# Performance work log

Hardware: AMD Instinct MI355X
Metric: run time of the kernel (lower is better)

## Reference

```python
import jax, jax.numpy as jnp
import numpy as np
from jax import lax

DG = 8          # deformable groups
KH = KW = 3
K = KH * KW
PAD = 1


def conv3x3(x, w, b):
    # x: (B,C,H,W), w: (O,C,3,3) -> SAME conv, stride 1
    y = lax.conv_general_dilated(x, w, (1, 1), ((PAD, PAD), (PAD, PAD)),
                                 dimension_numbers=('NCHW', 'OIHW', 'NCHW'))
    return y + b[None, :, None, None]


def lrelu(x):
    return jnp.where(x >= 0, x, 0.1 * x)


def modulated_deform_conv(x, offset, mask, w, b):
    """DCNv2 semantics: stride=1, pad=1, dilation=1, groups=1.
    x: (B,C,H,W); offset: (B, 2*DG*K, H, W); mask: (B, DG*K, H, W) (already sigmoided);
    w: (O, C, 3, 3); b: (O,).
    Offset channel layout per CUDA kernel: (DG, K, 2[y,x]).
    """
    B, C, H, W = x.shape
    cg = C // DG
    off = offset.reshape(B, DG, K, 2, H, W)
    dy, dx = off[:, :, :, 0], off[:, :, :, 1]            # (B,DG,K,H,W)

    ky, kx = jnp.meshgrid(jnp.arange(KH), jnp.arange(KW), indexing='ij')
    ky = ky.reshape(K).astype(x.dtype)
    kx = kx.reshape(K).astype(x.dtype)
    base_y = jnp.arange(H, dtype=x.dtype)[None, :, None] - PAD + ky[:, None, None]  # (K,H,1)
    base_x = jnp.arange(W, dtype=x.dtype)[None, None, :] - PAD + kx[:, None, None]  # (K,1,W)
    py = dy + base_y                                     # (B,DG,K,H,W)
    px = dx + base_x

    y0 = jnp.floor(py)
    x0 = jnp.floor(px)
    wy = py - y0
    wx = px - x0
    y0i = y0.astype(jnp.int32)
    x0i = x0.astype(jnp.int32)

    xg = x.reshape(B, DG, cg, H * W)

    def gather(yi, xi):
        valid = ((yi >= 0) & (yi < H) & (xi >= 0) & (xi < W)).astype(x.dtype)
        idx = jnp.clip(yi, 0, H - 1) * W + jnp.clip(xi, 0, W - 1)   # (B,DG,K,H,W)
        idxf = idx.reshape(B, DG, 1, K * H * W)
        vals = jnp.take_along_axis(xg, jnp.broadcast_to(idxf, (B, DG, cg, K * H * W)), axis=3)
        return vals.reshape(B, DG, cg, K, H, W) * valid[:, :, None]

    samp = gather(y0i, x0i) * ((1 - wy) * (1 - wx))[:, :, None]
    samp = samp + gather(y0i, x0i + 1) * ((1 - wy) * wx)[:, :, None]
    samp = samp + gather(y0i + 1, x0i) * (wy * (1 - wx))[:, :, None]
    samp = samp + gather(y0i + 1, x0i + 1) * (wy * wx)[:, :, None]

    samp = samp * mask.reshape(B, DG, 1, K, H, W)        # modulated
    wr = w.reshape(w.shape[0], DG, cg, K)
    out = jnp.einsum('odck,bdckhw->bohw', wr, samp)
    return out + b[None, :, None, None]


def dcn_pack(x, feat, off_w, off_b, w, b):
    # conv_offset on `feat` -> (B, 3*DG*K, H, W); chunk into o1,o2,mask
    out = conv3x3(feat, off_w, off_b)
    o1, o2, m = jnp.split(out, 3, axis=1)
    offset = jnp.concatenate([o1, o2], axis=1)
    mask = jax.nn.sigmoid(m)
    return modulated_deform_conv(x, offset, mask, w, b)


def setup_inputs() -> dict:
    key = jax.random.key(0)
    ks = jax.random.split(key, 24)
    B, C, H, W = 4, 64, 192, 192
    nf = C

    def wconv(k, o, i, s=0.02):
        return jax.random.normal(k, (o, i, 3, 3), jnp.float32) * s

    inp = {
        'nbr_l1': jax.random.normal(ks[0], (B, C, H, W), jnp.float32),
        'ref_l1': jax.random.normal(ks[1], (B, C, H, W), jnp.float32),
        'oc1_w': wconv(ks[2], nf, 2 * nf), 'oc1_b': jnp.zeros((nf,), jnp.float32),
        'oc2_w': wconv(ks[3], nf, nf), 'oc2_b': jnp.zeros((nf,), jnp.float32),
        'dcn1_off_w': wconv(ks[4], 3 * DG * K, nf, 0.01), 'dcn1_off_b': jnp.zeros((3 * DG * K,), jnp.float32),
        'dcn1_w': wconv(ks[5], nf, nf), 'dcn1_b': jnp.zeros((nf,), jnp.float32),
        'fc_w': wconv(ks[6], nf, nf), 'fc_b': jnp.zeros((nf,), jnp.float32),
        'cas1_w': wconv(ks[7], nf, 2 * nf), 'cas1_b': jnp.zeros((nf,), jnp.float32),
        'cas2_w': wconv(ks[8], nf, nf), 'cas2_b': jnp.zeros((nf,), jnp.float32),
        'casd_off_w': wconv(ks[9], 3 * DG * K, nf, 0.01), 'casd_off_b': jnp.zeros((3 * DG * K,), jnp.float32),
        'casd_w': wconv(ks[10], nf, nf), 'casd_b': jnp.zeros((nf,), jnp.float32),
    }
    return inp


def reference(nbr_l1, ref_l1, oc1_w, oc1_b, oc2_w, oc2_b,
              dcn1_off_w, dcn1_off_b, dcn1_w, dcn1_b, fc_w, fc_b,
              cas1_w, cas1_b, cas2_w, cas2_b,
              casd_off_w, casd_off_b, casd_w, casd_b):
    offset = jnp.concatenate([nbr_l1, ref_l1], axis=1)
    offset = lrelu(conv3x3(offset, oc1_w, oc1_b))
    offset = lrelu(conv3x3(offset, oc2_w, oc2_b))
    feat = dcn_pack(nbr_l1, offset, dcn1_off_w, dcn1_off_b, dcn1_w, dcn1_b)
    feat = conv3x3(feat, fc_w, fc_b)                     # no activation (matches source)
    offset = jnp.concatenate([feat, ref_l1], axis=1)
    offset = lrelu(conv3x3(lrelu(conv3x3(offset, cas1_w, cas1_b)), cas2_w, cas2_b))
    feat = lrelu(dcn_pack(feat, offset, casd_off_w, casd_off_b, casd_w, casd_b))
    return feat
```

## Files before the change

### kernel.cpp

```cpp
#include <hip/hip_runtime.h>
#include <hip/hip_bf16.h>
#include <math.h>

typedef __hip_bfloat16 bf16;
typedef float  floatx16 __attribute__((ext_vector_type(16)));
typedef short  short8   __attribute__((ext_vector_type(8)));

#define Bn 4
#define NF 64
#define Hn 192
#define Wn 192
#define HWn (Hn*Wn)

#define WA_OC1  0
#define WA_OC2  73728
#define WA_FC   110592
#define WA_CAS1 147456
#define WA_CAS2 221184
#define WA_D1O  258048
#define WA_CDO  405504
#define WP_D1   552960
#define WP_CD   589824
#define B_OC1  0
#define B_OC2  64
#define B_FC   128
#define B_CAS1 192
#define B_CAS2 256
#define B_D1O  320
#define B_CDO  536
#define B_D1P  752
#define B_CDP  816
#define BIAS_OFF  1024
#define WPOOL_OFF 5120
#define BUF_OFF   1261568
#define FEAT_BYTES 18874368

#define WROWS 12
#define WCOLS 12
#define WSTR  72
#define SSTR2 152

__device__ __forceinline__ float b2f(bf16 v){ return __bfloat162float(v); }
__device__ __forceinline__ bf16  f2b(float v){ return __float2bfloat16(v); }
__device__ __forceinline__ float us2f(unsigned short u){ return __uint_as_float(((unsigned)u) << 16); }
__device__ __forceinline__ float ld(const void* p, size_t i, int f32){
    if (f32) return ((const float*)p)[i];
    return b2f(((const bf16*)p)[i]);
}

union B8 { uint2 u2[2]; uint4 u4; short8 s8; };
union V8 { uint4 u4; unsigned short us[8]; bf16 h[8]; };
union V4 { uint2 u2; bf16 h[4]; };

struct P20 { const void* p[20]; int n[20]; };

__global__ void detect_bias(P20 a, int* __restrict__ flags, float* __restrict__ bp){
    __shared__ int sf[20];
    int t = threadIdx.x;
    if (t < 20){
        const unsigned short* u = (const unsigned short*)a.p[t];
        int n = a.n[t]; if (n > 512) n = 512;
        int f32 = 0;
        for (int i = 0; i < n; ++i){
            float v = __uint_as_float(((unsigned)u[i]) << 16);
            if (!(fabsf(v) < 1e3f)) f32 = 1;
        }
        sf[t] = f32; flags[t] = f32;
    }
    __syncthreads();
    const int src[9] = {3,5,11,13,15,7,17,9,19};
    const int off[9] = {B_OC1,B_OC2,B_FC,B_CAS1,B_CAS2,B_D1O,B_CDO,B_D1P,B_CDP};
    const int sz[9]  = {64,64,64,64,64,216,216,64,64};
    for (int s = 0; s < 9; ++s)
        if (t < sz[s]) bp[off[s] + t] = ld(a.p[src[s]], t, sf[src[s]]);
}

__global__ void prep_weights(P20 a, const int* __restrict__ flags, bf16* __restrict__ wp)
{
    const int srcI[9] = {2,4,10,12,14,6,16,8,18};
    const int dstO[9] = {WA_OC1,WA_OC2,WA_FC,WA_CAS1,WA_CAS2,WA_D1O,WA_CDO,WP_D1,WP_CD};
    const int cinA[9] = {128,64,64,128,64,64,64,0,0};
    const int coutA[9]= {64,64,64,64,64,216,216,0,0};
    const int nblk[9] = {288,144,144,288,144,576,576,144,144};

    int bx = blockIdx.x;
    int j = 0, base = 0;
    while (j < 8 && bx >= base + nblk[j]){ base += nblk[j]; ++j; }
    int idx = (bx - base)*256 + threadIdx.x;
    const void* src = a.p[srcI[j]];
    const int f = flags[srcI[j]];
    bf16* dst = wp + dstO[j];

    int jj = idx & 7;
    int ko = (idx>>3) & 1;
    int mm = (idx>>4) & 31;
    int rest = idx >> 9;
    if (cinA[j]){
        int KK = cinA[j] >> 4;
        int kk = rest % KK; rest /= KK;
        int tap = rest % 9;
        int ocb = rest / 9;
        int oc = ocb*32 + mm;
        int ci = kk*16 + ko*8 + jj;
        float v = 0.f;
        if (oc < coutA[j]) v = ld(src, ((size_t)oc*cinA[j] + ci)*9 + tap, f);
        dst[idx] = f2b(v);
    } else {
        int kk = rest % 36;
        int ocb = rest / 36;
        int oc = ocb*32 + mm;
        int kp   = kk*16 + ko*8 + jj;
        int slot = kp >> 3;
        int cg   = kp & 7;
        int dg   = slot / 9;
        int tap  = slot - dg*9;
        int k    = (dg*8 + cg)*9 + tap;
        dst[idx] = f2b(ld(src, (size_t)oc*576 + k, f));
    }
}

__global__ __launch_bounds__(256)
void pack_x(const void* __restrict__ src, const int* __restrict__ flags, int fi,
            bf16* __restrict__ dst)
{
    __shared__ bf16 s[64*65];
    const int b    = blockIdx.y;
    const int pix0 = blockIdx.x * 64;
    const int t    = threadIdx.x;
    const int f    = (fi >= 0) ? flags[fi] : 0;

    const int px8 = (t & 7) * 8;
    const int ci0 = t >> 3;
#pragma unroll
    for (int it = 0; it < 2; ++it){
        int ci = ci0 + it*32;
        size_t g = ((size_t)b*NF + ci)*HWn + pix0 + px8;
        if (f){
            float4 a0 = *(const float4*)((const float*)src + g);
            float4 a1 = *(const float4*)((const float*)src + g + 4);
            bf16* sp = &s[ci*65 + px8];
            sp[0]=f2b(a0.x); sp[1]=f2b(a0.y); sp[2]=f2b(a0.z); sp[3]=f2b(a0.w);
            sp[4]=f2b(a1.x); sp[5]=f2b(a1.y); sp[6]=f2b(a1.z); sp[7]=f2b(a1.w);
        } else {
            V8 v; v.u4 = *(const uint4*)((const bf16*)src + g);
            bf16* sp = &s[ci*65 + px8];
#pragma unroll
            for (int j = 0; j < 8; ++j) sp[j] = v.h[j];
        }
    }
    __syncthreads();

    const int px  = t >> 2;
    const int ch0 = (t & 3) * 16;
    V8 o0, o1;
#pragma unroll
    for (int j = 0; j < 8; ++j){
        o0.h[j] = s[(ch0 + j)*65 + px];
        o1.h[j] = s[(ch0 + 8 + j)*65 + px];
    }
    bf16* dp = dst + ((size_t)b*HWn + pix0 + px)*64 + ch0;
    *(uint4*)(dp)     = o0.u4;
    *(uint4*)(dp + 8) = o1.u4;
}

template<int KK, int NOCB>
__global__ __launch_bounds__(256, 2)
void conv_mfma(const bf16* __restrict__ inA, const bf16* __restrict__ inB,
               const bf16* __restrict__ wA, const float* __restrict__ bias,
               bf16* __restrict__ out, int ACT)
{
    constexpr int CinT  = KK*16;
    constexpr int ciPad = CinT + 4;
    constexpr int CH8   = CinT/8;
    constexpr int CSH   = (KK==4)?3:4;
    extern __shared__ __align__(16) char smem_raw[];
    bf16* s_in = (bf16*)smem_raw;

    const int b  = blockIdx.z;
    const int bx = blockIdx.x;
    const int ty = bx/3, tx = bx - ty*3;
    const int h0 = ty*2, x0 = tx*64;
    const int tid = threadIdx.x;

    for (int r = 0; r < 4; ++r){
        const int y = h0 - 1 + r;
        const bool yv = (unsigned)y < (unsigned)Hn;
        const size_t rb = ((size_t)b*HWn + (size_t)y*Wn)*64;
        for (int e = tid; e < 66*CH8; e += 256){
            const int c   = e >> CSH;
            const int ch8 = e & (CH8-1);
            const int x = x0 - 1 + c;
            B8 v; v.u4 = make_uint4(0,0,0,0);
            if (yv && (unsigned)x < (unsigned)Wn){
                if (KK==8 && ch8 >= 8) v.u4 = *(const uint4*)(inB + rb + (size_t)x*64 + (ch8-8)*8);
                else                   v.u4 = *(const uint4*)(inA + rb + (size_t)x*64 + ch8*8);
            }
            bf16* dp = &s_in[(size_t)(r*66 + c)*ciPad + ch8*8];
            *(uint2*)(dp)     = v.u2[0];
            *(uint2*)(dp + 4) = v.u2[1];
        }
    }
    __syncthreads();

    const int w    = tid >> 6;
    const int lane = tid & 63;
    const int m    = lane & 31;
    const int half = lane >> 5;
    const int och  = (w >> 1) * 32;
    const int rw   = (w & 1);
    const int gpx0 = (h0 + rw)*Wn + x0;

#pragma unroll
    for (int ot = 0; ot < NOCB; ++ot){
        const int ocb = ot*2 + (w >> 1);
        const bf16* wb = wA + ((size_t)ocb*9*KK)*512 + m*16 + half*8;

        floatx16 a0, a1;
#pragma unroll
        for (int r = 0; r < 16; ++r){ a0[r] = 0.f; a1[r] = 0.f; }

        B8 ring[2][4];
#pragma unroll
        for (int i = 0; i < 4; ++i) ring[0][i].u4 = *(const uint4*)(wb + (size_t)i*512);

        constexpr int NCH = 9*KK/4;
#pragma unroll
        for (int tap = 0; tap < 9; ++tap){
            const int ky = tap/3, kx = tap - 3*(tap/3);
            const bf16* s0 = s_in + (size_t)((ky+rw)*66 + kx + m)*ciPad + half*8;
#pragma unroll
            for (int hh = 0; hh < KK/4; ++hh){
                const int cidx = tap*(KK/4) + hh;
                const int cur = cidx & 1, nxt = cur ^ 1;
                if (cidx + 1 < NCH){
#pragma unroll
                    for (int i = 0; i < 4; ++i)
                        ring[nxt][i].u4 = *(const uint4*)(wb + (size_t)((cidx+1)*4 + i)*512);
                }
#pragma unroll
                for (int i = 0; i < 4; ++i){
                    const bf16* p0 = s0 + hh*64 + i*16;
                    const bf16* p1 = p0 + 32*ciPad;
                    B8 b0, b1;
                    b0.u2[0] = *(const uint2*)(p0); b0.u2[1] = *(const uint2*)(p0+4);
                    b1.u2[0] = *(const uint2*)(p1); b1.u2[1] = *(const uint2*)(p1+4);
                    a0 = __builtin_amdgcn_mfma_f32_32x32x16_bf16(ring[cur][i].s8, b0.s8, a0, 0,0,0);
                    a1 = __builtin_amdgcn_mfma_f32_32x32x16_bf16(ring[cur][i].s8, b1.s8, a1, 0,0,0);
                }
            }
        }

        if (ACT == 2){
#pragma unroll
            for (int s = 0; s < 2; ++s){
                const int px = gpx0 + s*32 + m;
#pragma unroll
                for (int r = 0; r < 16; ++r){
                    int row = (r & 3) + 8*(r >> 2) + 4*half;
                    int oc  = ot*64 + och + row;
                    if (oc < 216){
                        float v = (s ? a1[r] : a0[r]) + bias[oc];
                        if (oc >= 144) v = 1.f/(1.f + __expf(-v));
                        out[((size_t)b*216 + oc)*HWn + px] = f2b(v);
                    }
                }
            }
        } else {
#pragma unroll
            for (int s = 0; s < 2; ++s){
                const int px = gpx0 + s*32 + m;
                bf16* ob = out + ((size_t)b*HWn + px)*64 + och + 4*half;
#pragma unroll
                for (int q = 0; q < 4; ++q){
                    V4 u;
#pragma unroll
                    for (int j = 0; j < 4; ++j){
                        float v = (s ? a1[q*4+j] : a0[q*4+j]) + bias[och + 4*half + 8*q + j];
                        if (ACT == 1) v = (v >= 0.f) ? v : 0.1f*v;
                        u.h[j] = f2b(v);
                    }
                    *(uint2*)(ob + 8*q) = u.u2;
                }
            }
        }
    }
}

__global__ __launch_bounds__(256, 2)
void dcn_mfma(const bf16* __restrict__ xi,
              const bf16* __restrict__ offs,
              const bf16* __restrict__ wP,
              const float* __restrict__ pbias,
              void* __restrict__ out, int outF32, int ACT)
{
    __shared__ __align__(16) bf16 s_win[WROWS*WCOLS*WSTR];
    __shared__ __align__(16) bf16 s_samp[64*SSTR2];

    const int b   = blockIdx.y;
    const int bx  = blockIdx.x;
    const int tx  = bx % (Wn/8);
    const int ty  = bx / (Wn/8);
    const int gx0 = tx*8, gy0 = ty*8;
    const int wx0 = gx0 - 2, wy0 = gy0 - 2;
    const int tid = threadIdx.x;

    const bf16* xb = xi + (size_t)b*HWn*64;

    for (int c = tid; c < WROWS*WCOLS*8; c += 256){
        int ch4 = c & 7;
        int pxi = c >> 3;
        int gy  = wy0 + pxi/WCOLS;
        int gx  = wx0 + pxi%WCOLS;
        uint4 v = {0u,0u,0u,0u};
        if ((unsigned)gy < (unsigned)Hn && (unsigned)gx < (unsigned)Wn)
            v = *(const uint4*)(xb + ((size_t)gy*Wn + gx)*64 + ch4*8);
        *(uint4*)&s_win[pxi*WSTR + ch4*8] = v;
    }

    const int px   = tid & 63;
    const int wq   = tid >> 6;
    const int pr   = px >> 3, pc = px & 7;
    const int gy   = gy0 + pr, gx = gx0 + pc;
    const int m    = px & 31;
    const int half = px >> 5;
    const int och  = (wq >> 1) * 32;
    const int pxh  = (wq & 1) * 32;

    const size_t obase = (size_t)b*216*HWn + (size_t)gy*Wn + gx;
    const uint4 z4 = {0u,0u,0u,0u};

    const bf16* wPb  = wP + ((size_t)(wq>>1)*36)*512 + m*16 + half*8;
    const bf16* srow = s_samp + (pxh + m)*SSTR2 + half*8;

    floatx16 acc;
#pragma unroll
    for (int r = 0; r < 16; ++r) acc[r] = 0.f;

    for (int pass = 0; pass < 4; ++pass){
        __syncthreads();

#pragma unroll
        for (int ii = 0; ii < 5; ++ii){
            int sl = wq + ii*4;
            if (sl < 18){
                int dgl = sl / 9;
                int tap = sl - dgl*9;
                int dg  = pass*2 + dgl;
                int ky  = tap / 3;
                int kx  = tap - ky*3;
                float dy = b2f(offs[obase + (size_t)(dg*18 + tap*2    )*HWn]);
                float dx = b2f(offs[obase + (size_t)(dg*18 + tap*2 + 1)*HWn]);
                float mk = b2f(offs[obase + (size_t)(144 + dg*9 + tap )*HWn]);
                float py  = dy + (float)(gy - 1 + ky);
                float pxx = dx + (float)(gx - 1 + kx);
                float y0f = floorf(py), x0f = floorf(pxx);
                int   y0  = (int)y0f,   xi0 = (int)x0f;
                float wy  = py - y0f,   wx  = pxx - x0f;
                float w00 = (1.f-wy)*(1.f-wx)*mk, w01 = (1.f-wy)*wx*mk;
                float w10 = wy*(1.f-wx)*mk,       w11 = wy*wx*mk;
                int ly = y0 - wy0, lx = xi0 - wx0;

                auto fetch = [&](int ly_, int lx_, int y_, int x_) -> uint4 {
                    if ((unsigned)ly_ < (unsigned)WROWS && (unsigned)lx_ < (unsigned)WCOLS)
                        return *(const uint4*)&s_win[(ly_*WCOLS + lx_)*WSTR + dg*8];
                    if ((unsigned)y_ < (unsigned)Hn && (unsigned)x_ < (unsigned)Wn)
                        return *(const uint4*)(xb + ((size_t)y_*Wn + x_)*64 + dg*8);
                    return z4;
                };
                V8 c00, c01, c10, c11, o;
                c00.u4 = fetch(ly,   lx,   y0,   xi0  );
                c01.u4 = fetch(ly,   lx+1, y0,   xi0+1);
                c10.u4 = fetch(ly+1, lx,   y0+1, xi0  );
                c11.u4 = fetch(ly+1, lx+1, y0+1, xi0+1);
#pragma unroll
                for (int j = 0; j < 8; ++j){
                    float v = w00*us2f(c00.us[j]) + w01*us2f(c01.us[j])
                            + w10*us2f(c10.us[j]) + w11*us2f(c11.us[j]);
                    o.h[j] = f2b(v);
                }
                *(uint4*)&s_samp[px*SSTR2 + sl*8] = o.u4;
            }
        }
        __syncthreads();

#pragma unroll
        for (int kk = 0; kk < 9; ++kk){
            B8 ba; ba.u4 = *(const uint4*)(wPb + (size_t)(pass*9 + kk)*512);
            B8 bb; bb.u4 = *(const uint4*)(srow + kk*16);
            acc = __builtin_amdgcn_mfma_f32_32x32x16_bf16(ba.s8, bb.s8, acc, 0, 0, 0);
        }
    }

    const int opx = pxh + m;
    const int pxo = (gy0 + (opx >> 3))*Wn + gx0 + (opx & 7);
    if (outF32){
#pragma unroll
        for (int r = 0; r < 16; ++r){
            int row = (r & 3) + 8*(r >> 2) + 4*half;
            int oc  = och + row;
            float v = acc[r] + pbias[oc];
            if (ACT) v = (v >= 0.f) ? v : 0.1f*v;
            ((float*)out)[((size_t)b*NF + oc)*HWn + pxo] = v;
        }
    } else {
        bf16* ob = (bf16*)out + ((size_t)b*HWn + pxo)*64 + och + 4*half;
#pragma unroll
        for (int q = 0; q < 4; ++q){
            V4 u;
#pragma unroll
            for (int j = 0; j < 4; ++j){
                int oc = och + 4*half + 8*q + j;
                float v = acc[q*4 + j] + pbias[oc];
                if (ACT) v = (v >= 0.f) ? v : 0.1f*v;
                u.h[j] = f2b(v);
            }
            *(uint2*)(ob + 8*q) = u.u2;
        }
    }
}

extern "C" void kernel_launch(void* const* d_in, const int* in_sizes, int n_in,
                              void* d_out, int out_size, void* d_ws, size_t ws_size,
                              hipStream_t stream)
{
    enum { I_NBR=0, I_REF=1 };

    int*   flags = (int*)d_ws;
    float* bp    = (float*)((char*)d_ws + BIAS_OFF);
    bf16*  wp    = (bf16*) ((char*)d_ws + WPOOL_OFF);
    bf16*  t1    = (bf16*) ((char*)d_ws + BUF_OFF);
    bf16*  f1    = (bf16*) ((char*)d_ws + BUF_OFF + FEAT_BYTES);
    bf16*  offs  = (bf16*) ((char*)d_ws + BUF_OFF + 2*(size_t)FEAT_BYTES);
    bf16*  t0    = (bf16*) d_out;
    bf16*  nbr_i = (bf16*)((char*)d_out + FEAT_BYTES);
    bf16*  refA  = offs;
    bf16*  refB  = nbr_i;

    P20 a;
    for (int i = 0; i < 20; ++i){ a.p[i] = d_in[i]; a.n[i] = in_sizes[i]; }

    detect_bias<<<1, 256, 0, stream>>>(a, flags, bp);
    prep_weights<<<2448, 256, 0, stream>>>(a, flags, wp);

    dim3 blk(256,1,1);
    const int smem64  = 4*66*68*2;
    const int smem128 = 4*66*132*2;
    dim3 gC (288, 1, Bn);
    dim3 gD (576, Bn, 1);
    dim3 gP (576, Bn, 1);

    pack_x<<<gP, blk, 0, stream>>>(d_in[I_NBR], flags, I_NBR, nbr_i);
    pack_x<<<gP, blk, 0, stream>>>(d_in[I_REF], flags, I_REF, refA);
    conv_mfma<8,1><<<gC, blk, smem128, stream>>>(nbr_i, refA, wp+WA_OC1, bp+B_OC1, t0, 1);
    conv_mfma<4,1><<<gC, blk, smem64, stream>>>(t1==t1?t0:t0, nullptr, wp+WA_OC2, bp+B_OC2, t1, 1);
    conv_mfma<4,4><<<gC, blk, smem64, stream>>>(t1, nullptr, wp+WA_D1O, bp+B_D1O, offs, 2);
    dcn_mfma<<<gD, blk, 0, stream>>>(nbr_i, offs, wp+WP_D1, bp+B_D1P, t1, 0, 0);
    pack_x<<<gP, blk, 0, stream>>>(d_in[I_REF], flags, I_REF, refB);
    conv_mfma<4,1><<<gC, blk, smem64, stream>>>(t1, nullptr, wp+WA_FC, bp+B_FC, f1, 0);
    conv_mfma<8,1><<<gC, blk, smem128, stream>>>(f1, refB, wp+WA_CAS1, bp+B_CAS1, t0, 1);
    conv_mfma<4,1><<<gC, blk, smem64, stream>>>(t0, nullptr, wp+WA_CAS2, bp+B_CAS2, t1, 1);
    conv_mfma<4,4><<<gC, blk, smem64, stream>>>(t1, nullptr, wp+WA_CDO, bp+B_CDO, offs, 2);
    dcn_mfma<<<gD, blk, 0, stream>>>(f1, offs, wp+WP_CD, bp+B_CDP, d_out, 1, 1);
}
```

Measured before the change: 858.6 us.

## Stage conv weights through double-buffered LDS for 64-channel convolutions

For the KK=4 convolutions, each block now cooperatively copies the per-tap weight slice into a double-buffered LDS area and has waves read their A operands from LDS, instead of each wave streaming weights from global memory into registers. This is meant to cut redundant global weight traffic and latency across waves. The price is a __syncthreads per tap, extra LDS per block, and an unrolled loop turned into a runtime loop. The launch bounds also drop the minimum-blocks hint, which can change register allocation and occupancy.

After: 895.5 us. 4.3% more time.

```diff
diff --git a/kernel.cpp b/kernel.cpp
--- a/kernel.cpp
+++ b/kernel.cpp
@@ -163,8 +163,8 @@
     *(uint4*)(dp + 8) = o1.u4;
 }
 
-template<int KK, int NOCB>
-__global__ __launch_bounds__(256, 2)
+template<int KK, int NOCB, int WLDS>
+__global__ __launch_bounds__(256)
 void conv_mfma(const bf16* __restrict__ inA, const bf16* __restrict__ inB,
                const bf16* __restrict__ wA, const float* __restrict__ bias,
                bf16* __restrict__ out, int ACT)
@@ -175,6 +175,7 @@
     constexpr int CSH   = (KK==4)?3:4;
     extern __shared__ __align__(16) char smem_raw[];
     bf16* s_in = (bf16*)smem_raw;
+    bf16* s_w  = (bf16*)(smem_raw + 4*66*ciPad*2);
 
     const int b  = blockIdx.z;
     const int bx = blockIdx.x;
@@ -200,7 +201,6 @@
             *(uint2*)(dp + 4) = v.u2[1];
         }
     }
-    __syncthreads();
 
     const int w    = tid >> 6;
     const int lane = tid & 63;
@@ -209,63 +209,129 @@
     const int och  = (w >> 1) * 32;
     const int rw   = (w & 1);
     const int gpx0 = (h0 + rw)*Wn + x0;
-
-#pragma unroll
-    for (int ot = 0; ot < NOCB; ++ot){
-        const int ocb = ot*2 + (w >> 1);
-        const bf16* wb = wA + ((size_t)ocb*9*KK)*512 + m*16 + half*8;
-
+    const int osel = (w >> 1);
+
+    auto stage_w = [&](int c, int cur){
+        const int ot  = c/9, tap = c - 9*(c/9);
+        for (int e = tid; e < KK*128; e += 256){
+            const int os = e >> (KK==4?8:9);
+            const int wi = e & (KK*64 - 1);
+            const bf16* sp = wA + ((size_t)((ot*2 + os)*9 + tap)*KK)*512 + wi*8;
+            *(uint4*)&s_w[(size_t)(cur*2 + os)*(KK*512) + wi*8] = *(const uint4*)sp;
+        }
+    };
+
+    if (WLDS) stage_w(0, 0);
+    __syncthreads();
+
+    if (WLDS){
+        constexpr int NCH = NOCB*9;
         floatx16 a0, a1;
 #pragma unroll
         for (int r = 0; r < 16; ++r){ a0[r] = 0.f; a1[r] = 0.f; }
-
-        B8 ring[2][4];
-#pragma unroll
-        for (int i = 0; i < 4; ++i) ring[0][i].u4 = *(const uint4*)(wb + (size_t)i*512);
-
-        constexpr int NCH = 9*KK/4;
-#pragma unroll
-        for (int tap = 0; tap < 9; ++tap){
+        int ot = 0, tap = 0;
+
+        for (int c = 0; c < NCH; ++c){
+            const int cur = c & 1;
+            if (c + 1 < NCH) stage_w(c+1, cur ^ 1);
+
             const int ky = tap/3, kx = tap - 3*(tap/3);
             const bf16* s0 = s_in + (size_t)((ky+rw)*66 + kx + m)*ciPad + half*8;
-#pragma unroll
-            for (int hh = 0; hh < KK/4; ++hh){
-                const int cidx = tap*(KK/4) + hh;
-                const int cur = cidx & 1, nxt = cur ^ 1;
-                if (cidx + 1 < NCH){
-#pragma unroll
-                    for (int i = 0; i < 4; ++i)
-                        ring[nxt][i].u4 = *(const uint4*)(wb + (size_t)((cidx+1)*4 + i)*512);
+            const bf16* aw = s_w + (size_t)(cur*2 + osel)*(KK*512) + m*16 + half*8;
+#pragma unroll
+            for (int kk = 0; kk < KK; ++kk){
+                B8 ba; ba.u4 = *(const uint4*)(aw + kk*512);
+                const bf16* p0 = s0 + kk*16;
+                const bf16* p1 = p0 + 32*ciPad;
+                B8 b0, b1;
+                b0.u2[0] = *(const uint2*)(p0); b0.u2[1] = *(const uint2*)(p0+4);
+                b1.u2[0] = *(const uint2*)(p1); b1.u2[1] = *(const uint2*)(p1+4);
+                a0 = __builtin_amdgcn_mfma_f32_32x32x16_bf16(ba.s8, b0.s8, a0, 0,0,0);
+                a1 = __builtin_amdgcn_mfma_f32_32x32x16_bf16(ba.s8, b1.s8, a1, 0,0,0);
+            }
+
+            if (tap == 8){
+                if (ACT == 2){
+#pragma unroll
+                    for (int s = 0; s < 2; ++s){
+                        const int px = gpx0 + s*32 + m;
+#pragma unroll
+                        for (int r = 0; r < 16; ++r){
+                            int row = (r & 3) + 8*(r >> 2) + 4*half;
+                            int oc  = ot*64 + och + row;
+                            if (oc < 216){
+                                float v = (s ? a1[r] : a0[r]) + bias[oc];
+                                if (oc >= 144) v = 1.f/(1.f + __expf(-v));
+                                out[((size_t)b*216 + oc)*HWn + px] = f2b(v);
+                            }
+                        }
+                    }
+                } else {
+#pragma unroll
+                    for (int s = 0; s < 2; ++s){
+                        const int px = gpx0 + s*32 + m;
+                        bf16* ob = out + ((size_t)b*HWn + px)*64 + och + 4*half;
+#pragma unroll
+                        for (int q = 0; q < 4; ++q){
+                            V4 u;
+#pragma unroll
+                            for (int j = 0; j < 4; ++j){
+                                float v = (s ? a1[q*4+j] : a0[q*4+j]) + bias[och + 4*half + 8*q + j];
+                                if (ACT == 1) v = (v >= 0.f) ? v : 0.1f*v;
+                                u.h[j] = f2b(v);
+                            }
+                            *(uint2*)(ob + 8*q) = u.u2;
+                        }
+                    }
                 }
 #pragma unroll
-                for (int i = 0; i < 4; ++i){
-                    const bf16* p0 = s0 + hh*64 + i*16;
-                    const bf16* p1 = p0 + 32*ciPad;
-                    B8 b0, b1;
-                    b0.u2[0] = *(const uint2*)(p0); b0.u2[1] = *(const uint2*)(p0+4);
-                    b1.u2[0] = *(const uint2*)(p1); b1.u2[1] = *(const uint2*)(p1+4);
-                    a0 = __builtin_amdgcn_mfma_f32_32x32x16_bf16(ring[cur][i].s8, b0.s8, a0, 0,0,0);
-                    a1 = __builtin_amdgcn_mfma_f32_32x32x16_bf16(ring[cur][i].s8, b1.s8, a1, 0,0,0);
-                }
-            }
-        }
-
-        if (ACT == 2){
-#pragma unroll
-            for (int s = 0; s < 2; ++s){
-                const int px = gpx0 + s*32 + m;
-#pragma unroll
-                for (int r = 0; r < 16; ++r){
-                    int row = (r & 3) + 8*(r >> 2) + 4*half;
-                    int oc  = ot*64 + och + row;
-                    if (oc < 216){
-                        float v = (s ? a1[r] : a0[r]) + bias[oc];
-                        if (oc >= 144) v = 1.f/(1.f + __expf(-v));
-                        out[((size_t)b*216 + oc)*HWn + px] = f2b(v);
+                for (int r = 0; r < 16; ++r){ a0[r] = 0.f; a1[r] = 0.f; }
+                tap = 0; ++ot;
+            } else ++tap;
+
+            __syncthreads();
+        }
+    } else {
+#pragma unroll
+        for (int ot = 0; ot < NOCB; ++ot){
+            const int ocb = ot*2 + osel;
+            const bf16* wb = wA + ((size_t)ocb*9*KK)*512 + m*16 + half*8;
+
+            floatx16 a0, a1;
+#pragma unroll
+            for (int r = 0; r < 16; ++r){ a0[r] = 0.f; a1[r] = 0.f; }
+
+            B8 ring[2][4];
+#pragma unroll
+            for (int i = 0; i < 4; ++i) ring[0][i].u4 = *(const uint4*)(wb + (size_t)i*512);
+
+            constexpr int NCH = 9*KK/4;
+#pragma unroll
+            for (int tap = 0; tap < 9; ++tap){
+                const int ky = tap/3, kx = tap - 3*(tap/3);
+                const bf16* s0 = s_in + (size_t)((ky+rw)*66 + kx + m)*ciPad + half*8;
+#pragma unroll
+                for (int hh = 0; hh < KK/4; ++hh){
+                    const int cidx = tap*(KK/4) + hh;
+                    const int cur = cidx & 1, nxt = cur ^ 1;
+                    if (cidx + 1 < NCH){
+#pragma unroll
+                        for (int i = 0; i < 4; ++i)
+                            ring[nxt][i].u4 = *(const uint4*)(wb + (size_t)((cidx+1)*4 + i)*512);
+                    }
+#pragma unroll
+                    for (int i = 0; i < 4; ++i){
+                        const bf16* p0 = s0 + hh*64 + i*16;
+                        const bf16* p1 = p0 + 32*ciPad;
+                        B8 b0, b1;
+                        b0.u2[0] = *(const uint2*)(p0); b0.u2[1] = *(const uint2*)(p0+4);
+                        b1.u2[0] = *(const uint2*)(p1); b1.u2[1] = *(const uint2*)(p1+4);
+                        a0 = __builtin_amdgcn_mfma_f32_32x32x16_bf16(ring[cur][i].s8, b0.s8, a0, 0,0,0);
+                        a1 = __builtin_amdgcn_mfma_f32_32x32x16_bf16(ring[cur][i].s8, b1.s8, a1, 0,0,0);
                     }
                 }
             }
-        } else {
+
 #pragma unroll
             for (int s = 0; s < 2; ++s){
                 const int px = gpx0 + s*32 + m;
@@ -443,7 +509,7 @@
     prep_weights<<<2448, 256, 0, stream>>>(a, flags, wp);
 
     dim3 blk(256,1,1);
-    const int smem64  = 4*66*68*2;
+    const int smem64  = 4*66*68*2 + 2*2*4*512*2;
     const int smem128 = 4*66*132*2;
     dim3 gC (288, 1, Bn);
     dim3 gD (576, Bn, 1);
@@ -451,14 +517,14 @@
 
     pack_x<<<gP, blk, 0, stream>>>(d_in[I_NBR], flags, I_NBR, nbr_i);
     pack_x<<<gP, blk, 0, stream>>>(d_in[I_REF], flags, I_REF, refA);
-    conv_mfma<8,1><<<gC, blk, smem128, stream>>>(nbr_i, refA, wp+WA_OC1, bp+B_OC1, t0, 1);
-    conv_mfma<4,1><<<gC, blk, smem64, stream>>>(t1==t1?t0:t0, nullptr, wp+WA_OC2, bp+B_OC2, t1, 1);
-    conv_mfma<4,4><<<gC, blk, smem64, stream>>>(t1, nullptr, wp+WA_D1O, bp+B_D1O, offs, 2);
+    conv_mfma<8,1,0><<<gC, blk, smem128, stream>>>(nbr_i, refA, wp+WA_OC1, bp+B_OC1, t0, 1);
+    conv_mfma<4,1,1><<<gC, blk, smem64, stream>>>(t0, nullptr, wp+WA_OC2, bp+B_OC2, t1, 1);
+    conv_mfma<4,4,1><<<gC, blk, smem64, stream>>>(t1, nullptr, wp+WA_D1O, bp+B_D1O, offs, 2);
     dcn_mfma<<<gD, blk, 0, stream>>>(nbr_i, offs, wp+WP_D1, bp+B_D1P, t1, 0, 0);
     pack_x<<<gP, blk, 0, stream>>>(d_in[I_REF], flags, I_REF, refB);
-    conv_mfma<4,1><<<gC, blk, smem64, stream>>>(t1, nullptr, wp+WA_FC, bp+B_FC, f1, 0);
-    conv_mfma<8,1><<<gC, blk, smem128, stream>>>(f1, refB, wp+WA_CAS1, bp+B_CAS1, t0, 1);
-    conv_mfma<4,1><<<gC, blk, smem64, stream>>>(t0, nullptr, wp+WA_CAS2, bp+B_CAS2, t1, 1);
-    conv_mfma<4,4><<<gC, blk, smem64, stream>>>(t1, nullptr, wp+WA_CDO, bp+B_CDO, offs, 2);
+    conv_mfma<4,1,1><<<gC, blk, smem64, stream>>>(t1, nullptr, wp+WA_FC, bp+B_FC, f1, 0);
+    conv_mfma<8,1,0><<<gC, blk, smem128, stream>>>(f1, refB, wp+WA_CAS1, bp+B_CAS1, t0, 1);
+    conv_mfma<4,1,1><<<gC, blk, smem64, stream>>>(t0, nullptr, wp+WA_CAS2, bp+B_CAS2, t1, 1);
+    conv_mfma<4,4,1><<<gC, blk, smem64, stream>>>(t1, nullptr, wp+WA_CDO, bp+B_CDO, offs, 2);
     dcn_mfma<<<gD, blk, 0, stream>>>(f1, offs, wp+WP_CD, bp+B_CDP, d_out, 1, 1);
 }
```
